# Optimization experiments

Hardware: AMD Instinct MI355X
Metric: run time of the kernel (lower is better)

Reference implementation:

```python
import jax, jax.numpy as jnp
import numpy as np

D_MODEL = 512
NUM_HEADS = 8
D_K = D_MODEL // NUM_HEADS
LN_EPS = 1e-5


def setup_inputs() -> dict:
    key = jax.random.key(0)
    ks = jax.random.split(key, 11)
    d = D_MODEL
    s = 1.0 / np.sqrt(d)
    return {
        "x": jax.random.normal(ks[0], (4, 2048, d), dtype=jnp.float32),
        "Wq": jax.random.uniform(ks[1], (d, d), jnp.float32, -s, s),
        "bq": jax.random.uniform(ks[2], (d,), jnp.float32, -s, s),
        "Wk": jax.random.uniform(ks[3], (d, d), jnp.float32, -s, s),
        "bk": jax.random.uniform(ks[4], (d,), jnp.float32, -s, s),
        "Wv": jax.random.uniform(ks[5], (d, d), jnp.float32, -s, s),
        "bv": jax.random.uniform(ks[6], (d,), jnp.float32, -s, s),
        "Wo": jax.random.uniform(ks[7], (d, d), jnp.float32, -s, s),
        "bo": jax.random.uniform(ks[8], (d,), jnp.float32, -s, s),
        "gamma": jnp.ones((d,), jnp.float32),
        "beta": jnp.zeros((d,), jnp.float32),
    }


def reference(x, Wq, bq, Wk, bk, Wv, bv, Wo, bo, gamma, beta):
    # x: (B, S, D). Dropout is identity (eval mode).
    B, S, D = x.shape
    H, dk = NUM_HEADS, D_K
    # Linear layers use torch convention: y = x @ W.T + b
    q = (x @ Wq.T + bq).reshape(B, S, H, dk).transpose(0, 2, 1, 3)  # (B,H,S,dk)
    k = (x @ Wk.T + bk).reshape(B, S, H, dk).transpose(0, 2, 1, 3)
    v = (x @ Wv.T + bv).reshape(B, S, H, dk).transpose(0, 2, 1, 3)
    scores = jnp.einsum("bhqd,bhkd->bhqk", q, k) / jnp.sqrt(jnp.float32(dk))
    attn = jax.nn.softmax(scores, axis=-1)
    ctx = jnp.einsum("bhqk,bhkd->bhqd", attn, v)  # (B,H,S,dk)
    ctx = ctx.transpose(0, 2, 1, 3).reshape(B, S, D)
    out = ctx @ Wo.T + bo
    # residual + LayerNorm
    y = x + out
    mu = jnp.mean(y, axis=-1, keepdims=True)
    var = jnp.mean(jnp.square(y - mu), axis=-1, keepdims=True)
    return (y - mu) / jnp.sqrt(var + LN_EPS) * gamma + beta
```

## Files before the change

### kernel.cpp

```cpp
#include <hip/hip_runtime.h>
#include <math.h>

#define D 512
#define NH 8
#define DK 64
#define S 2048
#define BATCH 4
#define N_TOK (BATCH * S)

#define QSCALE 0.18033688f

typedef __bf16 bf16x8 __attribute__((ext_vector_type(8)));
typedef __bf16 bf16x4 __attribute__((ext_vector_type(4)));
typedef float f32x4 __attribute__((ext_vector_type(4)));

#define AS1 __attribute__((address_space(1)))
#define AS3 __attribute__((address_space(3)))

#define OFF_XB   0
#define OFF_WB   8388608
#define OFF_Q    10485760
#define OFF_K    18874368
#define OFF_VT   27262976
#define OFF_CTX  35651584
#define OFF_Y    10485760
#define OFF_FLAG 44040192

static __device__ __forceinline__ bf16x8 ldg8(const __bf16* p) {
    return *(const bf16x8*)p;
}
static __device__ __forceinline__ f32x4 mfma16(bf16x8 a, bf16x8 b, f32x4 c) {
    return __builtin_amdgcn_mfma_f32_16x16x32_bf16(a, b, c, 0, 0, 0);
}
static __device__ __forceinline__ float ldf(const void* p, size_t i, int isf) {
    return isf ? ((const float*)p)[i] : (float)(((const __bf16*)p)[i]);
}
static __device__ __forceinline__ unsigned bfbits(float x) {
    __bf16 b = (__bf16)x;
    return (unsigned)__builtin_bit_cast(unsigned short, b);
}
static __device__ __forceinline__ float fexp2(float x) {
#if __has_builtin(__builtin_amdgcn_exp2f)
    return __builtin_amdgcn_exp2f(x);
#else
    return exp2f(x);
#endif
}
static __device__ __forceinline__ void gload_lds16(const void* g, void* l) {
    __builtin_amdgcn_global_load_lds((const AS1 char*)g, (AS3 char*)l, 16, 0, 0);
}

__global__ __launch_bounds__(64)
void detect_kernel(const void* __restrict__ x, int* __restrict__ flag)
{
    const __bf16* p = (const __bf16*)x;
    const int l = threadIdx.x;
    int bad = 0;
#pragma unroll
    for (int j = 0; j < 32; ++j) {
        const float v = (float)p[l * 32 + j];
        bad |= !(fabsf(v) <= 64.0f);
    }
    const int any = (int)(__any(bad) ? 1 : 0);
    if (l == 0) *flag = any;
}

__global__ __launch_bounds__(256)
void cvt_kernel(const void* __restrict__ x,  const void* __restrict__ Wq,
                const void* __restrict__ Wk, const void* __restrict__ Wv,
                const void* __restrict__ Wo, __bf16* __restrict__ xb,
                __bf16* __restrict__ Wb, const int* __restrict__ flag)
{
    const int isf = *flag;
    const size_t i0 = ((size_t)blockIdx.x * 256 + threadIdx.x) * 8;
    const void* src;
    __bf16* dst;
    size_t off;
    if (i0 < 4194304) {
        src = x; off = i0; dst = xb + i0;
    } else {
        const size_t wrel = i0 - 4194304;
        const size_t w = wrel >> 18;
        src = (w == 0) ? Wq : (w == 1) ? Wk : (w == 2) ? Wv : Wo;
        off = wrel & 262143;
        dst = Wb + wrel;
    }
    bf16x8 r;
    if (isf) {
        const float* f = (const float*)src + off;
#pragma unroll
        for (int j = 0; j < 8; ++j) r[j] = (__bf16)f[j];
    } else {
        r = *(const bf16x8*)((const __bf16*)src + off);
    }
    *(bf16x8*)dst = r;
}

__global__ __launch_bounds__(256)
void qkv_kernel(const __bf16* __restrict__ xb, const __bf16* __restrict__ Wb,
                const void* __restrict__ bq, const void* __restrict__ bk,
                const void* __restrict__ bv, const int* __restrict__ flag,
                __bf16* __restrict__ Q, __bf16* __restrict__ K,
                __bf16* __restrict__ Vt)
{
    __shared__ __align__(16) char smem[16384];

    const int isf = *flag;
    const int tid = threadIdx.x;
    const int w = tid >> 6, l = tid & 63;
    const int lane16 = l & 15, quad = l >> 4;
    const int wm = w >> 1, wn = w & 1;
    const int m0 = blockIdx.x * 128;
    const int by = blockIdx.y;
    const int n0 = by * 128;

    const int cwl = w * 64 + l;
    const int g0 = (cwl & 3) ^ ((cwl >> 3) & 3);
    const __bf16* aS0 = xb + (size_t)(m0 + (cwl >> 2)) * D + g0 * 8;
    const __bf16* aS1 = aS0 + (size_t)64 * D;
    const __bf16* bS0 = Wb + (size_t)(n0 + (cwl >> 2)) * D + g0 * 8;
    const __bf16* bS1 = bS0 + (size_t)64 * D;

    const int sw = (quad ^ ((lane16 >> 1) & 3)) * 16;
    const int aoff = (wm * 64 + lane16) * 64 + sw;
    const int boff = 8192 + (wn * 64 + lane16) * 64 + sw;

    f32x4 acc[4][4];
#pragma unroll
    for (int i = 0; i < 4; ++i)
#pragma unroll
        for (int j = 0; j < 4; ++j) acc[i][j] = (f32x4){0,0,0,0};

    for (int kt = 0; kt < D / 32; ++kt) {
        gload_lds16(aS0 + kt * 32, smem + w * 1024);
        gload_lds16(aS1 + kt * 32, smem + 4096 + w * 1024);
        gload_lds16(bS0 + kt * 32, smem + 8192 + w * 1024);
        gload_lds16(bS1 + kt * 32, smem + 12288 + w * 1024);
        __syncthreads();

        bf16x8 af[4], bf[4];
#pragma unroll
        for (int i = 0; i < 4; ++i) af[i] = *(const bf16x8*)(smem + aoff + i * 1024);
#pragma unroll
        for (int j = 0; j < 4; ++j) bf[j] = *(const bf16x8*)(smem + boff + j * 1024);
#pragma unroll
        for (int i = 0; i < 4; ++i)
#pragma unroll
            for (int j = 0; j < 4; ++j)
                acc[i][j] = mfma16(af[i], bf[j], acc[i][j]);
        __syncthreads();
    }

    const int which = by >> 2;
    const int h = (by * 2 + wn) & 7;
    const float qs = (which == 0) ? QSCALE : 1.0f;
    const void* bias = (which == 0) ? bq : (which == 1) ? bk : bv;
    float bvv[4];
#pragma unroll
    for (int j = 0; j < 4; ++j)
        bvv[j] = ldf(bias, ((by & 3) * 128 + wn * 64 + 16 * j + lane16) & 511, isf);

    const int bb = m0 >> 11;
    const int ssb = (m0 & (S - 1)) + wm * 64;

    if (which < 2) {
        __bf16* out = ((which == 0) ? Q : K) + ((size_t)(bb * NH + h) * S) * DK;
#pragma unroll
        for (int i = 0; i < 4; ++i)
#pragma unroll
            for (int r = 0; r < 4; ++r) {
                const int ss = ssb + i * 16 + quad * 4 + r;
#pragma unroll
                for (int j = 0; j < 4; ++j)
                    out[(size_t)ss * DK + 16 * j + lane16] =
                        (__bf16)((acc[i][j][r] + bvv[j]) * qs);
            }
    } else {
#pragma unroll
        for (int i = 0; i < 4; ++i)
#pragma unroll
            for (int j = 0; j < 4; ++j) {
                const int dkc = 16 * j + lane16;
                __bf16* vp = Vt + ((size_t)(bb * NH + h) * DK + dkc) * S
                                + ssb + i * 16 + quad * 4;
                bf16x4 pkt;
#pragma unroll
                for (int r = 0; r < 4; ++r) pkt[r] = (__bf16)(acc[i][j][r] + bvv[j]);
                *(bf16x4*)vp = pkt;
            }
    }
}

__global__ __launch_bounds__(256)
void attn_kernel(const __bf16* __restrict__ Q, const __bf16* __restrict__ K,
                 const __bf16* __restrict__ Vt, __bf16* __restrict__ ctx)
{
    __shared__ __align__(16) char smem[49152];

    const int tid = threadIdx.x;
    const int w = tid >> 6, l = tid & 63;
    const int lane16 = l & 15, quad = l >> 4;

    const int lin = blockIdx.x;
    const int xcd = lin & 7;
    const int t = lin >> 3;
    const int bh = xcd * 4 + (t >> 4);
    const int qt = t & 15;
    const int b = bh >> 3, h = bh & 7;
    const size_t bhS = (size_t)bh * S;

    const int cwl = w * 64 + l;
    const char* kS[2];
    const char* vS[2];
#pragma unroll
    for (int c = 0; c < 2; ++c) {
        const int s = c * 256 + cwl;
        const int row = s >> 3;
        const int g = (s & 7) ^ (row & 7);
        kS[c] = (const char*)(K + (bhS + row) * DK) + g * 16;
        vS[c] = (const char*)(Vt + ((size_t)bh * DK + row) * S) + g * 16;
    }

    const int qbase = qt * 128 + w * 32;
    bf16x8 qa[2][2];
#pragma unroll
    for (int u = 0; u < 2; ++u) {
        const __bf16* Qp = Q + (bhS + qbase + u * 16 + lane16) * DK + quad * 8;
        qa[u][0] = ldg8(Qp);
        qa[u][1] = ldg8(Qp + 32);
    }

    const int x7 = lane16 & 7;
    char* pw = smem + 32768 + w * 4096;
    const int pwoff = lane16 * 128 + ((quad & 1) * 8);
    const int proff = lane16 * 128;

    f32x4 o[2][4];
#pragma unroll
    for (int u = 0; u < 2; ++u)
#pragma unroll
        for (int tt = 0; tt < 4; ++tt) o[u][tt] = (f32x4){0,0,0,0};
    float lp[2] = {0.f, 0.f};

    gload_lds16(kS[0], smem + w * 1024);
    gload_lds16(kS[1], smem + 4096 + w * 1024);
    gload_lds16(vS[0], smem + 8192 + w * 1024);
    gload_lds16(vS[1], smem + 12288 + w * 1024);

    for (int kc = 0; kc < S / 64; ++kc) {
        __syncthreads();

        const int buf = kc & 1;
        const char* kb = smem + buf * 16384;
        const char* vb = kb + 8192;

        if (kc + 1 < S / 64) {
            char* kb2 = smem + (buf ^ 1) * 16384;
            gload_lds16(kS[0] + (size_t)(kc + 1) * 8192, kb2 + w * 1024);
            gload_lds16(kS[1] + (size_t)(kc + 1) * 8192, kb2 + 4096 + w * 1024);
            gload_lds16(vS[0] + (size_t)(kc + 1) * 128, kb2 + 8192 + w * 1024);
            gload_lds16(vS[1] + (size_t)(kc + 1) * 128, kb2 + 12288 + w * 1024);
        }

        bf16x8 kfA[4], kfB[4];
#pragma unroll
        for (int tt = 0; tt < 4; ++tt) {
            const int base = (tt * 16 + lane16) * 128;
            kfA[tt] = *(const bf16x8*)(kb + base + ((quad ^ x7) * 16));
            kfB[tt] = *(const bf16x8*)(kb + base + (((quad + 4) ^ x7) * 16));
        }

#pragma unroll
        for (int u = 0; u < 2; ++u) {
            f32x4 st[4];
#pragma unroll
            for (int tt = 0; tt < 4; ++tt) {
                f32x4 z = {0,0,0,0};
                z = mfma16(kfA[tt], qa[u][0], z);
                st[tt] = mfma16(kfB[tt], qa[u][1], z);
            }
#pragma unroll
            for (int tt = 0; tt < 4; ++tt) {
                const float e0 = fexp2(st[tt][0]);
                const float e1 = fexp2(st[tt][1]);
                const float e2 = fexp2(st[tt][2]);
                const float e3 = fexp2(st[tt][3]);
                lp[u] += (e0 + e1) + (e2 + e3);
                uint2 pkt;
                pkt.x = bfbits(e0) | (bfbits(e1) << 16);
                pkt.y = bfbits(e2) | (bfbits(e3) << 16);
                *(uint2*)(pw + u * 2048 + pwoff
                          + (((tt * 2 + (quad >> 1)) ^ x7) * 16)) = pkt;
            }
        }

        bf16x8 vA[4], vB[4];
#pragma unroll
        for (int tt = 0; tt < 4; ++tt) {
            const int base = (tt * 16 + lane16) * 128;
            vA[tt] = *(const bf16x8*)(vb + base + ((quad ^ x7) * 16));
            vB[tt] = *(const bf16x8*)(vb + base + (((quad + 4) ^ x7) * 16));
        }
#pragma unroll
        for (int u = 0; u < 2; ++u) {
            const bf16x8 bp0 = *(const bf16x8*)(pw + u * 2048 + proff
                                                + (((0 + quad) ^ x7) * 16));
            const bf16x8 bp1 = *(const bf16x8*)(pw + u * 2048 + proff
                                                + (((4 + quad) ^ x7) * 16));
#pragma unroll
            for (int tt = 0; tt < 4; ++tt) {
                o[u][tt] = mfma16(vA[tt], bp0, o[u][tt]);
                o[u][tt] = mfma16(vB[tt], bp1, o[u][tt]);
            }
        }
    }

#pragma unroll
    for (int u = 0; u < 2; ++u) {
        float lsum = lp[u];
        lsum += __shfl_xor(lsum, 16);
        lsum += __shfl_xor(lsum, 32);
        const float inv = 1.0f / lsum;
        __bf16* cp = ctx + ((size_t)(b * S + qbase + u * 16 + lane16)) * D
                     + h * DK;
#pragma unroll
        for (int tt = 0; tt < 4; ++tt) {
            bf16x4 pkt;
#pragma unroll
            for (int r = 0; r < 4; ++r) pkt[r] = (__bf16)(o[u][tt][r] * inv);
            *(bf16x4*)(cp + tt * 16 + quad * 4) = pkt;
        }
    }
}

__global__ __launch_bounds__(256)
void proj_kernel(const __bf16* __restrict__ ctx, const __bf16* __restrict__ Wb,
                 const void* __restrict__ bo, const __bf16* __restrict__ xb,
                 const int* __restrict__ flag, __bf16* __restrict__ y)
{
    __shared__ __align__(16) char smem[12288];

    const int isf = *flag;
    const int tid = threadIdx.x;
    const int w = tid >> 6, l = tid & 63;
    const int lane16 = l & 15, quad = l >> 4;
    const int wm = w >> 1, wn = w & 1;
    const int m0 = blockIdx.x * 64;
    const int n0 = blockIdx.y * 128;

    const __bf16* Wo = Wb + (size_t)3 * 262144;
    const int cwl = w * 64 + l;
    const int g0 = (cwl & 3) ^ ((cwl >> 3) & 3);
    const __bf16* aS = ctx + (size_t)(m0 + (cwl >> 2)) * D + g0 * 8;
    const __bf16* bS0 = Wo + (size_t)(n0 + (cwl >> 2)) * D + g0 * 8;
    const __bf16* bS1 = bS0 + (size_t)64 * D;

    const int sw = (quad ^ ((lane16 >> 1) & 3)) * 16;
    const int aoff = (wm * 32 + lane16) * 64 + sw;
    const int boff = 4096 + (wn * 64 + lane16) * 64 + sw;

    f32x4 acc[2][4];
#pragma unroll
    for (int i = 0; i < 2; ++i)
#pragma unroll
        for (int j = 0; j < 4; ++j) acc[i][j] = (f32x4){0,0,0,0};

    for (int kt = 0; kt < D / 32; ++kt) {
        gload_lds16(aS + kt * 32, smem + w * 1024);
        gload_lds16(bS0 + kt * 32, smem + 4096 + w * 1024);
        gload_lds16(bS1 + kt * 32, smem + 8192 + w * 1024);
        __syncthreads();

        bf16x8 af[2], bf[4];
#pragma unroll
        for (int i = 0; i < 2; ++i) af[i] = *(const bf16x8*)(smem + aoff + i * 1024);
#pragma unroll
        for (int j = 0; j < 4; ++j) bf[j] = *(const bf16x8*)(smem + boff + j * 1024);
#pragma unroll
        for (int i = 0; i < 2; ++i)
#pragma unroll
            for (int j = 0; j < 4; ++j)
                acc[i][j] = mfma16(af[i], bf[j], acc[i][j]);
        __syncthreads();
    }

    float bvv[4];
#pragma unroll
    for (int j = 0; j < 4; ++j)
        bvv[j] = ldf(bo, n0 + wn * 64 + 16 * j + lane16, isf);

#pragma unroll
    for (int i = 0; i < 2; ++i)
#pragma unroll
        for (int r = 0; r < 4; ++r) {
            const int tok = m0 + wm * 32 + i * 16 + quad * 4 + r;
#pragma unroll
            for (int j = 0; j < 4; ++j) {
                const size_t idx = (size_t)tok * D + n0 + wn * 64 + 16 * j + lane16;
                y[idx] = (__bf16)(acc[i][j][r] + bvv[j] + (float)xb[idx]);
            }
        }
}

__global__ __launch_bounds__(64)
void ln_kernel(const __bf16* __restrict__ y, const void* __restrict__ gamma,
               const void* __restrict__ beta, const int* __restrict__ flag,
               void* __restrict__ out)
{
    const int isf = *flag;
    const int tok = blockIdx.x;
    const int l = threadIdx.x;
    const bf16x8 vv = ldg8(y + (size_t)tok * D + l * 8);

    float v[8];
    float sum = 0.f, sq = 0.f;
#pragma unroll
    for (int j = 0; j < 8; ++j) {
        v[j] = (float)vv[j];
        sum += v[j];
        sq  += v[j] * v[j];
    }
#pragma unroll
    for (int msk = 1; msk < 64; msk <<= 1) {
        sum += __shfl_xor(sum, msk);
        sq  += __shfl_xor(sq,  msk);
    }
    const float mean = sum * (1.0f / D);
    const float var  = sq * (1.0f / D) - mean * mean;
    const float rstd = rsqrtf(var + 1e-5f);

    const size_t base = (size_t)tok * D + l * 8;
#pragma unroll
    for (int j = 0; j < 8; ++j) {
        const float g  = ldf(gamma, l * 8 + j, isf);
        const float be = ldf(beta,  l * 8 + j, isf);
        const float r  = ((v[j] - mean) * rstd) * g + be;
        if (isf) ((float*)out)[base + j] = r;
        else     ((__bf16*)out)[base + j] = (__bf16)r;
    }
}

extern "C" void kernel_launch(void* const* d_in, const int* in_sizes, int n_in,
                              void* d_out, int out_size, void* d_ws,
                              size_t ws_size, hipStream_t stream)
{
    const void* x     = d_in[0];
    const void* Wq    = d_in[1];
    const void* bq    = d_in[2];
    const void* Wk    = d_in[3];
    const void* bk    = d_in[4];
    const void* Wv    = d_in[5];
    const void* bv    = d_in[6];
    const void* Wo    = d_in[7];
    const void* bo    = d_in[8];
    const void* gamma = d_in[9];
    const void* beta  = d_in[10];

    char* ws = (char*)d_ws;
    __bf16* xb  = (__bf16*)(ws + OFF_XB);
    __bf16* Wb  = (__bf16*)(ws + OFF_WB);
    __bf16* Qb  = (__bf16*)(ws + OFF_Q);
    __bf16* Kb  = (__bf16*)(ws + OFF_K);
    __bf16* Vtb = (__bf16*)(ws + OFF_VT);
    __bf16* ctx = (__bf16*)(ws + OFF_CTX);
    __bf16* y   = (__bf16*)(ws + OFF_Y);
    int*    flag = (int*)(ws + OFF_FLAG);

    detect_kernel<<<1, 64, 0, stream>>>(x, flag);
    cvt_kernel<<<5242880 / (256 * 8), 256, 0, stream>>>(
        x, Wq, Wk, Wv, Wo, xb, Wb, flag);
    qkv_kernel<<<dim3(N_TOK / 128, 12), 256, 0, stream>>>(
        xb, Wb, bq, bk, bv, flag, Qb, Kb, Vtb);
    attn_kernel<<<dim3(512), 256, 0, stream>>>(Qb, Kb, Vtb, ctx);
    proj_kernel<<<dim3(N_TOK / 64, 4), 256, 0, stream>>>(
        ctx, Wb, bo, xb, flag, y);
    ln_kernel<<<dim3(N_TOK), 64, 0, stream>>>(y, gamma, beta, flag, d_out);
}
```

Before: 195.8 us.

## Double-buffer GEMM loads, fold dtype detect, MFMA row sums, pack LN tokens

Double-buffers the LDS tiles in the QKV and output-projection GEMMs so the next K-slice loads while MFMAs run, and drops the second barrier per iteration. Folds the input dtype probe into the conversion kernel to remove one launch. The attention softmax denominator is now computed with an MFMA against a ones vector, using the bf16-truncated probabilities. Exp values are packed by truncation instead of rounding. LayerNorm processes four tokens per 256-thread block. The trade-offs are larger LDS use, which may lower occupancy, and slightly different numerics from truncation.

Result: faster. 191.0 us (-2.4%).

```diff
diff --git a/kernel.cpp b/kernel.cpp
--- a/kernel.cpp
+++ b/kernel.cpp
@@ -35,10 +35,6 @@
 static __device__ __forceinline__ float ldf(const void* p, size_t i, int isf) {
     return isf ? ((const float*)p)[i] : (float)(((const __bf16*)p)[i]);
 }
-static __device__ __forceinline__ unsigned bfbits(float x) {
-    __bf16 b = (__bf16)x;
-    return (unsigned)__builtin_bit_cast(unsigned short, b);
-}
 static __device__ __forceinline__ float fexp2(float x) {
 #if __has_builtin(__builtin_amdgcn_exp2f)
     return __builtin_amdgcn_exp2f(x);
@@ -46,32 +42,27 @@
     return exp2f(x);
 #endif
 }
+static __device__ __forceinline__ unsigned pack_trunc(float e0, float e1) {
+    return (__builtin_bit_cast(unsigned, e0) >> 16)
+         | (__builtin_bit_cast(unsigned, e1) & 0xFFFF0000u);
+}
 static __device__ __forceinline__ void gload_lds16(const void* g, void* l) {
     __builtin_amdgcn_global_load_lds((const AS1 char*)g, (AS3 char*)l, 16, 0, 0);
-}
-
-__global__ __launch_bounds__(64)
-void detect_kernel(const void* __restrict__ x, int* __restrict__ flag)
-{
-    const __bf16* p = (const __bf16*)x;
-    const int l = threadIdx.x;
-    int bad = 0;
-#pragma unroll
-    for (int j = 0; j < 32; ++j) {
-        const float v = (float)p[l * 32 + j];
-        bad |= !(fabsf(v) <= 64.0f);
-    }
-    const int any = (int)(__any(bad) ? 1 : 0);
-    if (l == 0) *flag = any;
 }
 
 __global__ __launch_bounds__(256)
 void cvt_kernel(const void* __restrict__ x,  const void* __restrict__ Wq,
                 const void* __restrict__ Wk, const void* __restrict__ Wv,
                 const void* __restrict__ Wo, __bf16* __restrict__ xb,
-                __bf16* __restrict__ Wb, const int* __restrict__ flag)
-{
-    const int isf = *flag;
+                __bf16* __restrict__ Wb, int* __restrict__ flag)
+{
+    const bf16x8 probe = ldg8((const __bf16*)x + (threadIdx.x & 63) * 8);
+    int bad = 0;
+#pragma unroll
+    for (int j = 0; j < 8; ++j) bad |= !(fabsf((float)probe[j]) <= 64.0f);
+    const int isf = __any(bad) ? 1 : 0;
+    if (blockIdx.x == 0 && threadIdx.x == 0) *flag = isf;
+
     const size_t i0 = ((size_t)blockIdx.x * 256 + threadIdx.x) * 8;
     const void* src;
     __bf16* dst;
@@ -103,7 +94,7 @@
                 __bf16* __restrict__ Q, __bf16* __restrict__ K,
                 __bf16* __restrict__ Vt)
 {
-    __shared__ __align__(16) char smem[16384];
+    __shared__ __align__(16) char smem[32768];
 
     const int isf = *flag;
     const int tid = threadIdx.x;
@@ -131,24 +122,33 @@
 #pragma unroll
         for (int j = 0; j < 4; ++j) acc[i][j] = (f32x4){0,0,0,0};
 
+    gload_lds16(aS0, smem + w * 1024);
+    gload_lds16(aS1, smem + 4096 + w * 1024);
+    gload_lds16(bS0, smem + 8192 + w * 1024);
+    gload_lds16(bS1, smem + 12288 + w * 1024);
+
     for (int kt = 0; kt < D / 32; ++kt) {
-        gload_lds16(aS0 + kt * 32, smem + w * 1024);
-        gload_lds16(aS1 + kt * 32, smem + 4096 + w * 1024);
-        gload_lds16(bS0 + kt * 32, smem + 8192 + w * 1024);
-        gload_lds16(bS1 + kt * 32, smem + 12288 + w * 1024);
         __syncthreads();
 
+        const char* bufp = smem + (kt & 1) * 16384;
+        if (kt + 1 < D / 32) {
+            char* nb = smem + ((kt + 1) & 1) * 16384;
+            gload_lds16(aS0 + (kt + 1) * 32, nb + w * 1024);
+            gload_lds16(aS1 + (kt + 1) * 32, nb + 4096 + w * 1024);
+            gload_lds16(bS0 + (kt + 1) * 32, nb + 8192 + w * 1024);
+            gload_lds16(bS1 + (kt + 1) * 32, nb + 12288 + w * 1024);
+        }
+
         bf16x8 af[4], bf[4];
 #pragma unroll
-        for (int i = 0; i < 4; ++i) af[i] = *(const bf16x8*)(smem + aoff + i * 1024);
-#pragma unroll
-        for (int j = 0; j < 4; ++j) bf[j] = *(const bf16x8*)(smem + boff + j * 1024);
+        for (int i = 0; i < 4; ++i) af[i] = *(const bf16x8*)(bufp + aoff + i * 1024);
+#pragma unroll
+        for (int j = 0; j < 4; ++j) bf[j] = *(const bf16x8*)(bufp + boff + j * 1024);
 #pragma unroll
         for (int i = 0; i < 4; ++i)
 #pragma unroll
             for (int j = 0; j < 4; ++j)
                 acc[i][j] = mfma16(af[i], bf[j], acc[i][j]);
-        __syncthreads();
     }
 
     const int which = by >> 2;
@@ -230,17 +230,22 @@
         qa[u][1] = ldg8(Qp + 32);
     }
 
+    bf16x8 aones;
+#pragma unroll
+    for (int j = 0; j < 8; ++j) aones[j] = (__bf16)1.0f;
+
     const int x7 = lane16 & 7;
     char* pw = smem + 32768 + w * 4096;
     const int pwoff = lane16 * 128 + ((quad & 1) * 8);
     const int proff = lane16 * 128;
 
-    f32x4 o[2][4];
-#pragma unroll
-    for (int u = 0; u < 2; ++u)
+    f32x4 o[2][4], lacc[2];
+#pragma unroll
+    for (int u = 0; u < 2; ++u) {
+        lacc[u] = (f32x4){0,0,0,0};
 #pragma unroll
         for (int tt = 0; tt < 4; ++tt) o[u][tt] = (f32x4){0,0,0,0};
-    float lp[2] = {0.f, 0.f};
+    }
 
     gload_lds16(kS[0], smem + w * 1024);
     gload_lds16(kS[1], smem + 4096 + w * 1024);
@@ -281,14 +286,9 @@
             }
 #pragma unroll
             for (int tt = 0; tt < 4; ++tt) {
-                const float e0 = fexp2(st[tt][0]);
-                const float e1 = fexp2(st[tt][1]);
-                const float e2 = fexp2(st[tt][2]);
-                const float e3 = fexp2(st[tt][3]);
-                lp[u] += (e0 + e1) + (e2 + e3);
                 uint2 pkt;
-                pkt.x = bfbits(e0) | (bfbits(e1) << 16);
-                pkt.y = bfbits(e2) | (bfbits(e3) << 16);
+                pkt.x = pack_trunc(fexp2(st[tt][0]), fexp2(st[tt][1]));
+                pkt.y = pack_trunc(fexp2(st[tt][2]), fexp2(st[tt][3]));
                 *(uint2*)(pw + u * 2048 + pwoff
                           + (((tt * 2 + (quad >> 1)) ^ x7) * 16)) = pkt;
             }
@@ -307,6 +307,8 @@
                                                 + (((0 + quad) ^ x7) * 16));
             const bf16x8 bp1 = *(const bf16x8*)(pw + u * 2048 + proff
                                                 + (((4 + quad) ^ x7) * 16));
+            lacc[u] = mfma16(aones, bp0, lacc[u]);
+            lacc[u] = mfma16(aones, bp1, lacc[u]);
 #pragma unroll
             for (int tt = 0; tt < 4; ++tt) {
                 o[u][tt] = mfma16(vA[tt], bp0, o[u][tt]);
@@ -317,10 +319,7 @@
 
 #pragma unroll
     for (int u = 0; u < 2; ++u) {
-        float lsum = lp[u];
-        lsum += __shfl_xor(lsum, 16);
-        lsum += __shfl_xor(lsum, 32);
-        const float inv = 1.0f / lsum;
+        const float inv = 1.0f / lacc[u][0];
         __bf16* cp = ctx + ((size_t)(b * S + qbase + u * 16 + lane16)) * D
                      + h * DK;
 #pragma unroll
@@ -338,7 +337,7 @@
                  const void* __restrict__ bo, const __bf16* __restrict__ xb,
                  const int* __restrict__ flag, __bf16* __restrict__ y)
 {
-    __shared__ __align__(16) char smem[12288];
+    __shared__ __align__(16) char smem[24576];
 
     const int isf = *flag;
     const int tid = threadIdx.x;
@@ -365,23 +364,31 @@
 #pragma unroll
         for (int j = 0; j < 4; ++j) acc[i][j] = (f32x4){0,0,0,0};
 
+    gload_lds16(aS, smem + w * 1024);
+    gload_lds16(bS0, smem + 4096 + w * 1024);
+    gload_lds16(bS1, smem + 8192 + w * 1024);
+
     for (int kt = 0; kt < D / 32; ++kt) {
-        gload_lds16(aS + kt * 32, smem + w * 1024);
-        gload_lds16(bS0 + kt * 32, smem + 4096 + w * 1024);
-        gload_lds16(bS1 + kt * 32, smem + 8192 + w * 1024);
         __syncthreads();
 
+        const char* bufp = smem + (kt & 1) * 12288;
+        if (kt + 1 < D / 32) {
+            char* nb = smem + ((kt + 1) & 1) * 12288;
+            gload_lds16(aS + (kt + 1) * 32, nb + w * 1024);
+            gload_lds16(bS0 + (kt + 1) * 32, nb + 4096 + w * 1024);
+            gload_lds16(bS1 + (kt + 1) * 32, nb + 8192 + w * 1024);
+        }
+
         bf16x8 af[2], bf[4];
 #pragma unroll
-        for (int i = 0; i < 2; ++i) af[i] = *(const bf16x8*)(smem + aoff + i * 1024);
-#pragma unroll
-        for (int j = 0; j < 4; ++j) bf[j] = *(const bf16x8*)(smem + boff + j * 1024);
+        for (int i = 0; i < 2; ++i) af[i] = *(const bf16x8*)(bufp + aoff + i * 1024);
+#pragma unroll
+        for (int j = 0; j < 4; ++j) bf[j] = *(const bf16x8*)(bufp + boff + j * 1024);
 #pragma unroll
         for (int i = 0; i < 2; ++i)
 #pragma unroll
             for (int j = 0; j < 4; ++j)
                 acc[i][j] = mfma16(af[i], bf[j], acc[i][j]);
-        __syncthreads();
     }
 
     float bvv[4];
@@ -402,14 +409,14 @@
         }
 }
 
-__global__ __launch_bounds__(64)
+__global__ __launch_bounds__(256)
 void ln_kernel(const __bf16* __restrict__ y, const void* __restrict__ gamma,
                const void* __restrict__ beta, const int* __restrict__ flag,
                void* __restrict__ out)
 {
     const int isf = *flag;
-    const int tok = blockIdx.x;
-    const int l = threadIdx.x;
+    const int l = threadIdx.x & 63;
+    const int tok = blockIdx.x * 4 + (threadIdx.x >> 6);
     const bf16x8 vv = ldg8(y + (size_t)tok * D + l * 8);
 
     float v[8];
@@ -466,7 +473,6 @@
     __bf16* y   = (__bf16*)(ws + OFF_Y);
     int*    flag = (int*)(ws + OFF_FLAG);
 
-    detect_kernel<<<1, 64, 0, stream>>>(x, flag);
     cvt_kernel<<<5242880 / (256 * 8), 256, 0, stream>>>(
         x, Wq, Wk, Wv, Wo, xb, Wb, flag);
     qkv_kernel<<<dim3(N_TOK / 128, 12), 256, 0, stream>>>(
@@ -474,5 +480,5 @@
     attn_kernel<<<dim3(512), 256, 0, stream>>>(Qb, Kb, Vtb, ctx);
     proj_kernel<<<dim3(N_TOK / 64, 4), 256, 0, stream>>>(
         ctx, Wb, bo, xb, flag, y);
-    ln_kernel<<<dim3(N_TOK), 64, 0, stream>>>(y, gamma, beta, flag, d_out);
-}
+    ln_kernel<<<dim3(N_TOK / 4), 256, 0, stream>>>(y, gamma, beta, flag, d_out);
+}
```
